# Kernel optimization log

Hardware: AMD Instinct MI355X
Metric: run time of the kernel (lower is better)

Reference implementation:

```python
import jax, jax.numpy as jnp
import numpy as np

EPS = 1e-5

def batchnorm2d(x, gamma, beta):
    # training-mode BN over (N, T, V) per channel; x: [N, C, T, V]
    mean = jnp.mean(x, axis=(0, 2, 3), keepdims=True)
    var = jnp.var(x, axis=(0, 2, 3), keepdims=True)
    xhat = (x - mean) * jax.lax.rsqrt(var + EPS)
    return xhat * gamma[None, :, None, None] + beta[None, :, None, None]

def temporal_shift(x, theta, stride):
    # learnable per-channel temporal shift with linear interpolation, zero pad
    # x: [N, C, T, V], theta: [C]
    N, C, T, V = x.shape
    T_out = T // stride
    t = jnp.arange(T_out, dtype=theta.dtype)
    pos = t[None, :] * stride + theta[:, None]          # [C, T_out]
    i0 = jnp.floor(pos).astype(jnp.int32)
    frac = (pos - i0.astype(theta.dtype))[None, :, :, None]  # [1,C,T_out,1]
    cidx = jnp.arange(C)[:, None]                        # [C, 1]

    def gather(idx):
        valid = (idx >= 0) & (idx < T)
        g = x[:, cidx, jnp.clip(idx, 0, T - 1), :]       # [N, C, T_out, V]
        return jnp.where(valid[None, :, :, None], g, 0.0)

    return gather(i0) * (1.0 - frac) + gather(i0 + 1) * frac

def setup_inputs() -> dict:
    key = jax.random.key(0)
    k = jax.random.split(key, 6)
    N, Cin, Cout, T, V = 64, 256, 256, 64, 25
    x = jax.random.normal(k[0], (N, Cin, T, V), dtype=jnp.float32)
    # kaiming normal fan_out for 1x1 conv: std = sqrt(2 / (Cout*1*1))
    conv_w = jax.random.normal(k[1], (Cout, Cin), dtype=jnp.float32) * np.float32(np.sqrt(2.0 / Cout))
    conv_b = jnp.zeros((Cout,), dtype=jnp.float32)
    bn1_g = jnp.ones((Cin,), dtype=jnp.float32)
    bn1_b = jnp.zeros((Cin,), dtype=jnp.float32)
    bn2_g = jnp.ones((Cin,), dtype=jnp.float32)   # bn_init(bn2, 1)
    bn2_b = jnp.zeros((Cin,), dtype=jnp.float32)
    theta_in = jax.random.uniform(k[2], (Cin,), jnp.float32, -1.0, 1.0)
    theta_out = jax.random.uniform(k[3], (Cout,), jnp.float32, -1.0, 1.0)
    return {"x": x, "conv_w": conv_w, "conv_b": conv_b,
            "bn1_g": bn1_g, "bn1_b": bn1_b, "bn2_g": bn2_g, "bn2_b": bn2_b,
            "theta_in": theta_in, "theta_out": theta_out}

def reference(x, conv_w, conv_b, bn1_g, bn1_b, bn2_g, bn2_b, theta_in, theta_out):
    stride = 1
    h = batchnorm2d(x, bn1_g, bn1_b)
    h = temporal_shift(h, theta_in, 1)
    h = jnp.einsum('nctv,oc->notv', h, conv_w) + conv_b[None, :, None, None]
    h = jax.nn.relu(h)
    h = temporal_shift(h, theta_out, stride)
    h = batchnorm2d(h, bn2_g, bn2_b)
    return h
```

## Files before the change

kernel.cpp:

```cpp
#include <hip/hip_runtime.h>


#define EPSV 1e-5f
constexpr int Nn = 64, Cc = 256, Tt = 64, Vv = 25;
constexpr int TV = Tt * Vv;
constexpr int CTV = Cc * TV;
constexpr float Minv = 1.0f / (Nn * TV);

typedef short short8 __attribute__((ext_vector_type(8)));
typedef float floatx4 __attribute__((ext_vector_type(4)));

__device__ __forceinline__ unsigned short f2bf(float f) {
    unsigned int u = __builtin_bit_cast(unsigned int, f);
    u += 0x7FFFu + ((u >> 16) & 1u);
    return (unsigned short)(u >> 16);
}
__device__ __forceinline__ float bflo(unsigned int w) {
    return __builtin_bit_cast(float, w << 16);
}
__device__ __forceinline__ float bfhi(unsigned int w) {
    return __builtin_bit_cast(float, w & 0xFFFF0000u);
}
__device__ __forceinline__ void unp8v(uint4 u, float* o) {
    o[0] = bflo(u.x); o[1] = bfhi(u.x); o[2] = bflo(u.y); o[3] = bfhi(u.y);
    o[4] = bflo(u.z); o[5] = bfhi(u.z); o[6] = bflo(u.w); o[7] = bfhi(u.w);
}
__device__ __forceinline__ void gload_lds16(const void* g, void* l) {
    __builtin_amdgcn_global_load_lds((const __attribute__((address_space(1))) void*)g,
                                     (__attribute__((address_space(3))) void*)l, 16, 0, 0);
}

__global__ __launch_bounds__(256) void k_stats_shift(const float* __restrict__ x,
                                                     const float* __restrict__ theta,
                                                     float* __restrict__ sacc,
                                                     float* __restrict__ qacc,
                                                     unsigned short* __restrict__ ht) {
    int c0 = blockIdx.x * 64;
    int E0 = blockIdx.y * 200;
    int n  = blockIdx.z;
    int tid = threadIdx.x;
    __shared__ __attribute__((aligned(16))) unsigned short xt[256][70];
    __shared__ int   pd[64];
    __shared__ float pf[64];
    if (tid < 64) {
        float th = theta[c0 + tid];
        float fd = floorf(th);
        pd[tid] = (int)fd;
        pf[tid] = th - fd;
    }
    int lo = E0 - 28; if (lo < 0) lo = 0;
    int hi = E0 + 228; if (hi > 1600) hi = 1600;
    int ldsoff = lo - (E0 - 28);
    int nf4 = (hi - lo) >> 2;
    {
        int cp = tid >> 3, li = tid & 7;
        int ca = 2 * cp;
        const float4* xr0 = (const float4*)(x + (size_t)n * CTV + (size_t)(c0 + ca) * TV + lo);
        const float4* xr1 = xr0 + (TV >> 2);
        float s0 = 0.f, q0 = 0.f, s1 = 0.f, q1 = 0.f;
        float4 acur = xr0[li], bcur = xr1[li];
#pragma unroll
        for (int s = 0; s < 8; ++s) {
            int i = li + s * 8;
            int inx = i + 8;
            float4 anxt, bnxt;
            if (inx < nf4) { anxt = xr0[inx]; bnxt = xr1[inx]; }
            if (i < nf4) {
                int r = ldsoff + i * 4;
#pragma unroll
                for (int k = 0; k < 4; ++k) {
                    float a = ((const float*)&acur)[k];
                    float b = ((const float*)&bcur)[k];
                    if ((unsigned)(r + k - 28) < 200u) {
                        s0 += a; q0 += a * a; s1 += b; q1 += b * b;
                    }
                    unsigned int pk = (unsigned int)f2bf(a) | (((unsigned int)f2bf(b)) << 16);
                    *(unsigned int*)&xt[r + k][ca] = pk;
                }
            }
            acur = anxt; bcur = bnxt;
        }
        for (int off = 4; off; off >>= 1) {
            s0 += __shfl_down(s0, off); q0 += __shfl_down(q0, off);
            s1 += __shfl_down(s1, off); q1 += __shfl_down(q1, off);
        }
        if (li == 0) {
            atomicAdd(&sacc[c0 + ca], s0);     atomicAdd(&qacc[c0 + ca], q0);
            atomicAdd(&sacc[c0 + ca + 1], s1); atomicAdd(&qacc[c0 + ca + 1], q1);
        }
    }
    __syncthreads();
    int cseg = tid & 7, er = tid >> 3;
    int cb = cseg * 8;
    int dk[8]; float fk[8];
#pragma unroll
    for (int k = 0; k < 8; ++k) { dk[k] = pd[cb + k]; fk[k] = pf[cb + k]; }
    for (int it = 0; it < 7; ++it) {
        int tv_l = er + it * 32;
        if (tv_l >= 200) break;
        int e = E0 + tv_l;
        float A8[8], B8[8], C8[8];
        {
            const unsigned short* rA = &xt[tv_l + 3][cb];
            const unsigned short* rB = &xt[tv_l + 28][cb];
            const unsigned short* rC = &xt[tv_l + 53][cb];
            uint2 a0 = *(const uint2*)rA, a1 = *(const uint2*)(rA + 4);
            uint2 b0 = *(const uint2*)rB, b1 = *(const uint2*)(rB + 4);
            uint2 g0 = *(const uint2*)rC, g1 = *(const uint2*)(rC + 4);
            A8[0]=bflo(a0.x); A8[1]=bfhi(a0.x); A8[2]=bflo(a0.y); A8[3]=bfhi(a0.y);
            A8[4]=bflo(a1.x); A8[5]=bfhi(a1.x); A8[6]=bflo(a1.y); A8[7]=bfhi(a1.y);
            B8[0]=bflo(b0.x); B8[1]=bfhi(b0.x); B8[2]=bflo(b0.y); B8[3]=bfhi(b0.y);
            B8[4]=bflo(b1.x); B8[5]=bfhi(b1.x); B8[6]=bflo(b1.y); B8[7]=bfhi(b1.y);
            C8[0]=bflo(g0.x); C8[1]=bfhi(g0.x); C8[2]=bflo(g0.y); C8[3]=bfhi(g0.y);
            C8[4]=bflo(g1.x); C8[5]=bfhi(g1.x); C8[6]=bflo(g1.y); C8[7]=bfhi(g1.y);
        }
        unsigned int w4[4];
#pragma unroll
        for (int k = 0; k < 8; ++k) {
            int d = dk[k]; float f = fk[k];
            float x0 = (d < 0) ? A8[k] : B8[k];
            float x1 = (d < 0) ? B8[k] : C8[k];
            int e0 = e + 25 * d;
            float v0 = ((unsigned)e0 < 1600u) ? x0 : 0.f;
            float v1 = ((unsigned)(e0 + 25) < 1600u) ? x1 : 0.f;
            unsigned short hb = f2bf(v0 + f * (v1 - v0));
            if (k & 1) w4[k >> 1] |= ((unsigned int)hb) << 16;
            else       w4[k >> 1] = hb;
        }
        uint4 st = { w4[0], w4[1], w4[2], w4[3] };
        *(uint4*)(ht + (size_t)(n * 1600 + e) * 256 + c0 + cb) = st;
    }
}

__global__ __launch_bounds__(256) void k_params(const float* __restrict__ w,
                                                const float* __restrict__ bias,
                                                const float* __restrict__ sacc,
                                                const float* __restrict__ qacc,
                                                const float* __restrict__ g,
                                                const float* __restrict__ b,
                                                const float* __restrict__ theta,
                                                unsigned short* __restrict__ wb,
                                                float* __restrict__ b2all,
                                                float* __restrict__ s0v,
                                                float* __restrict__ s63v) {
    int o = blockIdx.x, c = threadIdx.x;
    float mean = sacc[c] * Minv;
    float var  = qacc[c] * Minv - mean * mean;
    float sc = g[c] * rsqrtf(var + EPSV);
    float tc = b[c] - mean * sc;
    float th = theta[c];
    float fd = floorf(th);
    int d = (int)fd;
    float f = th - fd;
    float wv = w[o * 256 + c];
    wb[o * 256 + c] = f2bf(wv * sc);
    float wtc = wv * tc;
    float r0  = (d < 0) ? wtc * (1.f - f) : 0.f;
    float r63 = (d == 0) ? wtc * f : 0.f;
    for (int off = 32; off; off >>= 1) {
        wtc += __shfl_down(wtc, off);
        r0  += __shfl_down(r0, off);
        r63 += __shfl_down(r63, off);
    }
    __shared__ float aux[3][4];
    if ((c & 63) == 0) { int wi = c >> 6; aux[0][wi] = wtc; aux[1][wi] = r0; aux[2][wi] = r63; }
    __syncthreads();
    if (c == 0) {
        b2all[o] = bias[o] + aux[0][0] + aux[0][1] + aux[0][2] + aux[0][3];
        s0v[o]  = aux[1][0] + aux[1][1] + aux[1][2] + aux[1][3];
        s63v[o] = aux[2][0] + aux[2][1] + aux[2][2] + aux[2][3];
    }
}

__global__ __launch_bounds__(256, 2) void k_gemm(const unsigned short* __restrict__ ht,
                                                 const unsigned short* __restrict__ wb,
                                                 const float* __restrict__ b2all,
                                                 const float* __restrict__ s0v,
                                                 const float* __restrict__ s63v,
                                                 unsigned short* __restrict__ y) {
    int j0 = blockIdx.x * 128;
    int tid = threadIdx.x;
    int w = tid >> 6, lane = tid & 63;
    int quad = lane >> 4, l16 = lane & 15;
    __shared__ __attribute__((aligned(16))) unsigned short smem[36864];
    floatx4 acc[4][8] = {};
    int sg = (lane & 3) ^ ((lane >> 3) & 3);
    const unsigned short* wpA = wb + (size_t)(w * 64 + (lane >> 2)) * 256 + sg * 8;
    const unsigned short* hpB = ht + (size_t)(j0 + w * 32 + (lane >> 2)) * 256 + sg * 8;
    int rg = quad ^ ((l16 >> 1) & 3);

#define STAGE(buf, k0)                                                              \
    {                                                                               \
        unsigned short* Ab_ = smem + (buf) * 12288;                                 \
        unsigned short* Bb_ = Ab_ + 8192;                                           \
        _Pragma("unroll")                                                           \
        for (int a = 0; a < 4; ++a)                                                 \
            gload_lds16(wpA + (size_t)a * 16 * 256 + (k0), Ab_ + (w * 64 + a * 16) * 32); \
        _Pragma("unroll")                                                           \
        for (int b = 0; b < 2; ++b)                                                 \
            gload_lds16(hpB + (size_t)b * 16 * 256 + (k0), Bb_ + (w * 32 + b * 16) * 32); \
    }
#define COMPUTE(buf)                                                                \
    {                                                                               \
        const unsigned short* Ab_ = smem + (buf) * 12288;                           \
        const unsigned short* Bb_ = Ab_ + 8192;                                     \
        short8 af[4];                                                               \
        _Pragma("unroll")                                                           \
        for (int m = 0; m < 4; ++m)                                                 \
            af[m] = *(const short8*)&Ab_[(w * 64 + m * 16 + l16) * 32 + rg * 8];    \
        __builtin_amdgcn_s_setprio(1);                                              \
        _Pragma("unroll")                                                           \
        for (int jt = 0; jt < 8; ++jt) {                                            \
            short8 bfr = *(const short8*)&Bb_[(jt * 16 + l16) * 32 + rg * 8];       \
            _Pragma("unroll")                                                       \
            for (int m = 0; m < 4; ++m)                                             \
                acc[m][jt] = __builtin_amdgcn_mfma_f32_16x16x32_bf16(af[m], bfr, acc[m][jt], 0, 0, 0); \
        }                                                                           \
        __builtin_amdgcn_s_setprio(0);                                              \
    }
#define WAITVM(n) asm volatile("s_waitcnt vmcnt(" #n ")" ::: "memory")
#define BAR() __builtin_amdgcn_s_barrier()

    STAGE(0, 0)
    STAGE(1, 32)
    WAITVM(6); BAR();
    STAGE(2, 64)
    COMPUTE(0)
    WAITVM(6); BAR();
    STAGE(0, 96)
    COMPUTE(1)
    WAITVM(6); BAR();
    STAGE(1, 128)
    COMPUTE(2)
    WAITVM(6); BAR();
    STAGE(2, 160)
    COMPUTE(0)
    WAITVM(6); BAR();
    STAGE(0, 192)
    COMPUTE(1)
    WAITVM(6); BAR();
    STAGE(1, 224)
    COMPUTE(2)
    WAITVM(6); BAR();
    COMPUTE(0)
    WAITVM(0); BAR();
    COMPUTE(1)
#undef STAGE
#undef COMPUTE
#undef WAITVM
#undef BAR

    __syncthreads();
    unsigned short* Cl = smem;
    int li = tid & 15, orow = tid >> 4;
#pragma unroll
    for (int p = 0; p < 2; ++p) {
        if ((w >> 1) == p) {
            int rowbase = (w & 1) * 64;
#pragma unroll
            for (int m = 0; m < 4; ++m) {
                int ob = p * 128 + (w & 1) * 64 + m * 16 + quad * 4;
#pragma unroll
                for (int r = 0; r < 4; ++r) {
                    int o = ob + r;
                    float bb = b2all[o], e0 = s0v[o], e63 = s63v[o];
                    int lrow = rowbase + m * 16 + quad * 4 + r;
#pragma unroll
                    for (int jt = 0; jt < 8; ++jt) {
                        int jj = j0 + jt * 16;
                        int nn = jj / 1600;
                        int tvb = jj - nn * 1600 + l16;
                        float bia = bb - (tvb < 25 ? e0 : 0.f) - (tvb >= 1575 ? e63 : 0.f);
                        float v = acc[m][jt][r] + bia;
                        v = v > 0.f ? v : 0.f;
                        Cl[lrow * 136 + jt * 16 + l16] = f2bf(v);
                    }
                }
            }
        }
        __syncthreads();
#pragma unroll
        for (int pass = 0; pass < 8; ++pass) {
            int ol = orow + pass * 16;
            uint4 vv = *(const uint4*)&Cl[ol * 136 + li * 8];
            int o = p * 128 + ol;
            int j = j0 + li * 8;
            int nn = j / 1600;
            int tv = j - nn * 1600;
            *(uint4*)(y + (size_t)nn * CTV + (size_t)o * TV + tv) = vv;
        }
        if (p == 0) __syncthreads();
    }
}

__global__ __launch_bounds__(256) void k_bn2_stats(const unsigned short* __restrict__ y,
                                                   float* __restrict__ acc7) {
    int o = blockIdx.y, ng = blockIdx.x, tid = threadIdx.x;
    float S = 0.f, Q = 0.f, P = 0.f, Y0 = 0.f, Q0 = 0.f, Y63 = 0.f, Q63 = 0.f;
    if (tid < 200) {
        int e = tid * 8;
        int eB = e + 24; if (eB > 1592) eB = 1592;
        int eC = e + 32; if (eC > 1592) eC = 1592;
        const unsigned short* base0 = y + (size_t)(ng * 8) * CTV + (size_t)o * TV;
        uint4 ua = *(const uint4*)(base0 + e);
        uint4 ub = *(const uint4*)(base0 + eB);
        uint4 uc = *(const uint4*)(base0 + eC);
        for (int nn = 0; nn < 8; ++nn) {
            uint4 na, nb, nc;
            if (nn < 7) {
                const unsigned short* row = base0 + (size_t)(nn + 1) * CTV;
                na = *(const uint4*)(row + e);
                nb = *(const uint4*)(row + eB);
                nc = *(const uint4*)(row + eC);
            }
            float a[8], b[8], c[8];
            unp8v(ua, a); unp8v(ub, b); unp8v(uc, c);
#pragma unroll
            for (int k = 0; k < 8; ++k) {
                float v = a[k];
                S += v; Q += v * v;
                float vn = (k < 7) ? b[k + 1] : c[0];
                if (e + k < 1575) P += v * vn;
            }
            if (e < 32) {
#pragma unroll
                for (int k = 0; k < 8; ++k)
                    if (e + k < 25) { Y0 += a[k]; Q0 += a[k] * a[k]; }
            }
            if (e >= 1568) {
#pragma unroll
                for (int k = 0; k < 8; ++k)
                    if (e + k >= 1575) { Y63 += a[k]; Q63 += a[k] * a[k]; }
            }
            ua = na; ub = nb; uc = nc;
        }
    }
    for (int off = 32; off; off >>= 1) {
        S += __shfl_down(S, off); Q += __shfl_down(Q, off); P += __shfl_down(P, off);
        Y0 += __shfl_down(Y0, off); Q0 += __shfl_down(Q0, off);
        Y63 += __shfl_down(Y63, off); Q63 += __shfl_down(Q63, off);
    }
    if ((tid & 63) == 0) {
        atomicAdd(&acc7[o], S);           atomicAdd(&acc7[256 + o], Q);
        atomicAdd(&acc7[512 + o], P);     atomicAdd(&acc7[768 + o], Y0);
        atomicAdd(&acc7[1024 + o], Q0);   atomicAdd(&acc7[1280 + o], Y63);
        atomicAdd(&acc7[1536 + o], Q63);
    }
}

__global__ __launch_bounds__(256) void k_bn2_apply(const unsigned short* __restrict__ y,
                                                   const float* __restrict__ theta,
                                                   const float* __restrict__ acc7,
                                                   const float* __restrict__ g,
                                                   const float* __restrict__ b,
                                                   float* __restrict__ out) {
    int o = blockIdx.y, n = blockIdx.x, tid = threadIdx.x;
    float th = theta[o];
    float fd = floorf(th);
    int d = (int)fd;
    float f = th - fd;
    float S = acc7[o], Q = acc7[256 + o], P = acc7[512 + o];
    float Y0 = acc7[768 + o], Q0 = acc7[1024 + o], Y63 = acc7[1280 + o], Q63 = acc7[1536 + o];
    float omf = 1.f - f;
    float sz, qz;
    if (d < 0) { sz = S - omf * Y63; qz = omf * omf * (Q - Q63) + f * f * Q + 2.f * f * omf * P; }
    else       { sz = S - f * Y0;    qz = omf * omf * Q + f * f * (Q - Q0) + 2.f * f * omf * P; }
    float mean = sz * Minv;
    float var = qz * Minv - mean * mean;
    float sc = g[o] * rsqrtf(var + EPSV);
    float tc = b[o] - mean * sc;
    if (tid >= 200) return;
    int e = tid * 8;
    const unsigned short* row = y + (size_t)n * CTV + (size_t)o * TV;
    float a0[8], a1[8];
    if (d < 0) {
        int eA = e - 32; if (eA < 0) eA = 0;
        int eB = e - 24; if (eB < 0) eB = 0;
        float A[8], B[8], M[8];
        unp8v(*(const uint4*)(row + eA), A);
        unp8v(*(const uint4*)(row + eB), B);
        unp8v(*(const uint4*)(row + e), M);
        a0[0] = (e >= 25) ? A[7] : 0.f;
#pragma unroll
        for (int k = 1; k < 8; ++k) a0[k] = (e + k >= 25) ? B[k - 1] : 0.f;
#pragma unroll
        for (int k = 0; k < 8; ++k) a1[k] = M[k];
    } else {
        int eB = e + 24; if (eB > 1592) eB = 1592;
        int eC = e + 32; if (eC > 1592) eC = 1592;
        float M[8], B[8], C[8];
        unp8v(*(const uint4*)(row + e), M);
        unp8v(*(const uint4*)(row + eB), B);
        unp8v(*(const uint4*)(row + eC), C);
#pragma unroll
        for (int k = 0; k < 8; ++k) a0[k] = M[k];
#pragma unroll
        for (int k = 0; k < 7; ++k) a1[k] = (e + k < 1575) ? B[k + 1] : 0.f;
        a1[7] = (e + 7 < 1575) ? C[0] : 0.f;
    }
    float4 r0, r1;
#pragma unroll
    for (int k = 0; k < 4; ++k) {
        ((float*)&r0)[k] = (omf * a0[k] + f * a1[k]) * sc + tc;
        ((float*)&r1)[k] = (omf * a0[k + 4] + f * a1[k + 4]) * sc + tc;
    }
    float* op = out + (size_t)n * CTV + (size_t)o * TV + e;
    *(float4*)op = r0;
    *(float4*)(op + 4) = r1;
}

extern "C" void kernel_launch(void* const* d_in, const int* in_sizes, int n_in,
                              void* d_out, int out_size, void* d_ws, size_t ws_size,
                              hipStream_t stream) {
    const float* x      = (const float*)d_in[0];
    const float* conv_w = (const float*)d_in[1];
    const float* conv_b = (const float*)d_in[2];
    const float* bn1_g  = (const float*)d_in[3];
    const float* bn1_b  = (const float*)d_in[4];
    const float* bn2_g  = (const float*)d_in[5];
    const float* bn2_b  = (const float*)d_in[6];
    const float* th_in  = (const float*)d_in[7];
    const float* th_out = (const float*)d_in[8];
    float* out = (float*)d_out;

    char* ws = (char*)d_ws;
    unsigned short* ht = (unsigned short*)ws;
    unsigned short* yy = (unsigned short*)(ws + 52428800);
    unsigned short* wb = (unsigned short*)(ws + 104857600);
    float* sacc1 = (float*)(ws + 104988672);
    float* qacc1 = sacc1 + 256;
    float* acc7  = qacc1 + 256;
    float* b2all = acc7 + 7 * 256;
    float* s0v   = b2all + 256;
    float* s63v  = s0v + 256;

    hipMemsetAsync((void*)sacc1, 0, 9 * 256 * sizeof(float), stream);
    hipLaunchKernelGGL(k_stats_shift, dim3(4, 8, 64), dim3(256), 0, stream,
                       x, th_in, sacc1, qacc1, ht);
    hipLaunchKernelGGL(k_params, dim3(256), dim3(256), 0, stream,
                       conv_w, conv_b, sacc1, qacc1, bn1_g, bn1_b, th_in,
                       wb, b2all, s0v, s63v);
    hipLaunchKernelGGL(k_gemm, dim3(800), dim3(256), 0, stream,
                       ht, wb, b2all, s0v, s63v, yy);
    hipLaunchKernelGGL(k_bn2_stats, dim3(8, 256), dim3(256), 0, stream, yy, acc7);
    hipLaunchKernelGGL(k_bn2_apply, dim3(64, 256), dim3(256), 0, stream,
                       yy, th_out, acc7, bn2_g, bn2_b, out);
}
```

Measured before the change: 347.1 us.

## Store shifted activations channel-major and transpose via ds_read_b64_tr_b16 in GEMM

The first kernel no longer transposes x through LDS into a [n,tv,c] bf16 buffer. It streams each (n,c) row directly, applies the temporal shift with neighbouring global loads, and writes a channel-major [c, n*tv] bf16 buffer. The GEMM then loads B tiles from that layout and transposes them on the fly with ds_read_b64_tr_b16 LDS reads. The goal is to drop the LDS transpose and its strided writes from the stats/shift stage. The cost is more redundant global reads for the shift neighbours and a more complex inline-asm B-fragment path in the GEMM.

```diff
diff --git a/kernel.cpp b/kernel.cpp
--- a/kernel.cpp
+++ b/kernel.cpp
@@ -5,10 +5,13 @@
 constexpr int Nn = 64, Cc = 256, Tt = 64, Vv = 25;
 constexpr int TV = Tt * Vv;
 constexpr int CTV = Cc * TV;
+constexpr int NJ = Nn * TV;
 constexpr float Minv = 1.0f / (Nn * TV);
 
 typedef short short8 __attribute__((ext_vector_type(8)));
 typedef float floatx4 __attribute__((ext_vector_type(4)));
+typedef unsigned int uintx2 __attribute__((ext_vector_type(2)));
+typedef unsigned int uintx4 __attribute__((ext_vector_type(4)));
 
 __device__ __forceinline__ unsigned short f2bf(float f) {
     unsigned int u = __builtin_bit_cast(unsigned int, f);
@@ -30,105 +33,68 @@
                                      (__attribute__((address_space(3))) void*)l, 16, 0, 0);
 }
 
-__global__ __launch_bounds__(256) void k_stats_shift(const float* __restrict__ x,
-                                                     const float* __restrict__ theta,
-                                                     float* __restrict__ sacc,
-                                                     float* __restrict__ qacc,
-                                                     unsigned short* __restrict__ ht) {
-    int c0 = blockIdx.x * 64;
-    int E0 = blockIdx.y * 200;
-    int n  = blockIdx.z;
-    int tid = threadIdx.x;
-    __shared__ __attribute__((aligned(16))) unsigned short xt[256][70];
-    __shared__ int   pd[64];
-    __shared__ float pf[64];
-    if (tid < 64) {
-        float th = theta[c0 + tid];
-        float fd = floorf(th);
-        pd[tid] = (int)fd;
-        pf[tid] = th - fd;
-    }
-    int lo = E0 - 28; if (lo < 0) lo = 0;
-    int hi = E0 + 228; if (hi > 1600) hi = 1600;
-    int ldsoff = lo - (E0 - 28);
-    int nf4 = (hi - lo) >> 2;
-    {
-        int cp = tid >> 3, li = tid & 7;
-        int ca = 2 * cp;
-        const float4* xr0 = (const float4*)(x + (size_t)n * CTV + (size_t)(c0 + ca) * TV + lo);
-        const float4* xr1 = xr0 + (TV >> 2);
-        float s0 = 0.f, q0 = 0.f, s1 = 0.f, q1 = 0.f;
-        float4 acur = xr0[li], bcur = xr1[li];
-#pragma unroll
-        for (int s = 0; s < 8; ++s) {
-            int i = li + s * 8;
-            int inx = i + 8;
-            float4 anxt, bnxt;
-            if (inx < nf4) { anxt = xr0[inx]; bnxt = xr1[inx]; }
-            if (i < nf4) {
-                int r = ldsoff + i * 4;
-#pragma unroll
-                for (int k = 0; k < 4; ++k) {
-                    float a = ((const float*)&acur)[k];
-                    float b = ((const float*)&bcur)[k];
-                    if ((unsigned)(r + k - 28) < 200u) {
-                        s0 += a; q0 += a * a; s1 += b; q1 += b * b;
-                    }
-                    unsigned int pk = (unsigned int)f2bf(a) | (((unsigned int)f2bf(b)) << 16);
-                    *(unsigned int*)&xt[r + k][ca] = pk;
-                }
-            }
-            acur = anxt; bcur = bnxt;
-        }
-        for (int off = 4; off; off >>= 1) {
-            s0 += __shfl_down(s0, off); q0 += __shfl_down(q0, off);
-            s1 += __shfl_down(s1, off); q1 += __shfl_down(q1, off);
-        }
-        if (li == 0) {
-            atomicAdd(&sacc[c0 + ca], s0);     atomicAdd(&qacc[c0 + ca], q0);
-            atomicAdd(&sacc[c0 + ca + 1], s1); atomicAdd(&qacc[c0 + ca + 1], q1);
-        }
-    }
-    __syncthreads();
-    int cseg = tid & 7, er = tid >> 3;
-    int cb = cseg * 8;
-    int dk[8]; float fk[8];
-#pragma unroll
-    for (int k = 0; k < 8; ++k) { dk[k] = pd[cb + k]; fk[k] = pf[cb + k]; }
-    for (int it = 0; it < 7; ++it) {
-        int tv_l = er + it * 32;
-        if (tv_l >= 200) break;
-        int e = E0 + tv_l;
-        float A8[8], B8[8], C8[8];
-        {
-            const unsigned short* rA = &xt[tv_l + 3][cb];
-            const unsigned short* rB = &xt[tv_l + 28][cb];
-            const unsigned short* rC = &xt[tv_l + 53][cb];
-            uint2 a0 = *(const uint2*)rA, a1 = *(const uint2*)(rA + 4);
-            uint2 b0 = *(const uint2*)rB, b1 = *(const uint2*)(rB + 4);
-            uint2 g0 = *(const uint2*)rC, g1 = *(const uint2*)(rC + 4);
-            A8[0]=bflo(a0.x); A8[1]=bfhi(a0.x); A8[2]=bflo(a0.y); A8[3]=bfhi(a0.y);
-            A8[4]=bflo(a1.x); A8[5]=bfhi(a1.x); A8[6]=bflo(a1.y); A8[7]=bfhi(a1.y);
-            B8[0]=bflo(b0.x); B8[1]=bfhi(b0.x); B8[2]=bflo(b0.y); B8[3]=bfhi(b0.y);
-            B8[4]=bflo(b1.x); B8[5]=bfhi(b1.x); B8[6]=bflo(b1.y); B8[7]=bfhi(b1.y);
-            C8[0]=bflo(g0.x); C8[1]=bfhi(g0.x); C8[2]=bflo(g0.y); C8[3]=bfhi(g0.y);
-            C8[4]=bflo(g1.x); C8[5]=bfhi(g1.x); C8[6]=bflo(g1.y); C8[7]=bfhi(g1.y);
+__global__ __launch_bounds__(256) void k_bn1_stream(const float* __restrict__ x,
+                                                    const float* __restrict__ theta,
+                                                    float* __restrict__ sacc,
+                                                    float* __restrict__ qacc,
+                                                    unsigned short* __restrict__ ht2) {
+    int n = blockIdx.x, c = blockIdx.y, tid = threadIdx.x;
+    const float* xr = x + (size_t)n * CTV + (size_t)c * TV;
+    float th = theta[c];
+    float fd = floorf(th);
+    int d = (int)fd;
+    float f = th - fd, omf = 1.f - f;
+    float s = 0.f, q = 0.f;
+    if (tid < 200) {
+        int e = tid * 8;
+        float4 m0 = *(const float4*)(xr + e);
+        float4 m1 = *(const float4*)(xr + e + 4);
+        float M[8] = {m0.x, m0.y, m0.z, m0.w, m1.x, m1.y, m1.z, m1.w};
+#pragma unroll
+        for (int k = 0; k < 8; ++k) { s += M[k]; q += M[k] * M[k]; }
+        float out[8];
+        if (d < 0) {
+            int b0 = e - 28; if (b0 < 0) b0 = 0;
+            int b1 = e - 24; if (b1 < 0) b1 = 0;
+            int b2 = e - 20; if (b2 < 0) b2 = 0;
+            float4 l0 = *(const float4*)(xr + b0);
+            float4 l1 = *(const float4*)(xr + b1);
+            float4 l2 = *(const float4*)(xr + b2);
+            float S[8] = { l0.w, l1.x, l1.y, l1.z, l1.w, l2.x, l2.y, l2.z };
+#pragma unroll
+            for (int k = 0; k < 8; ++k) {
+                float v0 = (e + k >= 25) ? S[k] : 0.f;
+                out[k] = omf * v0 + f * M[k];
+            }
+        } else {
+            int b0 = e + 24; if (b0 > 1596) b0 = 1596;
+            int b1 = e + 28; if (b1 > 1596) b1 = 1596;
+            int b2 = e + 32; if (b2 > 1596) b2 = 1596;
+            float4 l0 = *(const float4*)(xr + b0);
+            float4 l1 = *(const float4*)(xr + b1);
+            float4 l2 = *(const float4*)(xr + b2);
+            float S[8] = { l0.y, l0.z, l0.w, l1.x, l1.y, l1.z, l1.w, l2.x };
+#pragma unroll
+            for (int k = 0; k < 8; ++k) {
+                float v1 = (e + k < 1575) ? S[k] : 0.f;
+                out[k] = omf * M[k] + f * v1;
+            }
         }
         unsigned int w4[4];
 #pragma unroll
-        for (int k = 0; k < 8; ++k) {
-            int d = dk[k]; float f = fk[k];
-            float x0 = (d < 0) ? A8[k] : B8[k];
-            float x1 = (d < 0) ? B8[k] : C8[k];
-            int e0 = e + 25 * d;
-            float v0 = ((unsigned)e0 < 1600u) ? x0 : 0.f;
-            float v1 = ((unsigned)(e0 + 25) < 1600u) ? x1 : 0.f;
-            unsigned short hb = f2bf(v0 + f * (v1 - v0));
-            if (k & 1) w4[k >> 1] |= ((unsigned int)hb) << 16;
-            else       w4[k >> 1] = hb;
-        }
+        for (int k = 0; k < 8; k += 2)
+            w4[k >> 1] = (unsigned)f2bf(out[k]) | (((unsigned)f2bf(out[k + 1])) << 16);
         uint4 st = { w4[0], w4[1], w4[2], w4[3] };
-        *(uint4*)(ht + (size_t)(n * 1600 + e) * 256 + c0 + cb) = st;
+        *(uint4*)(ht2 + (size_t)c * NJ + n * TV + e) = st;
+    }
+    for (int off = 32; off; off >>= 1) { s += __shfl_down(s, off); q += __shfl_down(q, off); }
+    __shared__ float red[8];
+    int wv = tid >> 6;
+    if ((tid & 63) == 0) { red[wv] = s; red[4 + wv] = q; }
+    __syncthreads();
+    if (tid == 0) {
+        atomicAdd(&sacc[c], red[0] + red[1] + red[2] + red[3]);
+        atomicAdd(&qacc[c], red[4] + red[5] + red[6] + red[7]);
     }
 }
 
@@ -172,7 +138,7 @@
     }
 }
 
-__global__ __launch_bounds__(256, 2) void k_gemm(const unsigned short* __restrict__ ht,
+__global__ __launch_bounds__(256, 2) void k_gemm(const unsigned short* __restrict__ ht2,
                                                  const unsigned short* __restrict__ wb,
                                                  const float* __restrict__ b2all,
                                                  const float* __restrict__ s0v,
@@ -186,60 +152,105 @@
     floatx4 acc[4][8] = {};
     int sg = (lane & 3) ^ ((lane >> 3) & 3);
     const unsigned short* wpA = wb + (size_t)(w * 64 + (lane >> 2)) * 256 + sg * 8;
-    const unsigned short* hpB = ht + (size_t)(j0 + w * 32 + (lane >> 2)) * 256 + sg * 8;
     int rg = quad ^ ((l16 >> 1) & 3);
-
-#define STAGE(buf, k0)                                                              \
-    {                                                                               \
-        unsigned short* Ab_ = smem + (buf) * 12288;                                 \
-        unsigned short* Bb_ = Ab_ + 8192;                                           \
-        _Pragma("unroll")                                                           \
-        for (int a = 0; a < 4; ++a)                                                 \
-            gload_lds16(wpA + (size_t)a * 16 * 256 + (k0), Ab_ + (w * 64 + a * 16) * 32); \
-        _Pragma("unroll")                                                           \
-        for (int b = 0; b < 2; ++b)                                                 \
-            gload_lds16(hpB + (size_t)b * 16 * 256 + (k0), Bb_ + (w * 32 + b * 16) * 32); \
-    }
-#define COMPUTE(buf)                                                                \
-    {                                                                               \
-        const unsigned short* Ab_ = smem + (buf) * 12288;                           \
-        const unsigned short* Bb_ = Ab_ + 8192;                                     \
-        short8 af[4];                                                               \
-        _Pragma("unroll")                                                           \
-        for (int m = 0; m < 4; ++m)                                                 \
-            af[m] = *(const short8*)&Ab_[(w * 64 + m * 16 + l16) * 32 + rg * 8];    \
-        __builtin_amdgcn_s_setprio(1);                                              \
-        _Pragma("unroll")                                                           \
-        for (int jt = 0; jt < 8; ++jt) {                                            \
-            short8 bfr = *(const short8*)&Bb_[(jt * 16 + l16) * 32 + rg * 8];       \
-            _Pragma("unroll")                                                       \
-            for (int m = 0; m < 4; ++m)                                             \
-                acc[m][jt] = __builtin_amdgcn_mfma_f32_16x16x32_bf16(af[m], bfr, acc[m][jt], 0, 0, 0); \
-        }                                                                           \
-        __builtin_amdgcn_s_setprio(0);                                              \
+    int brow0 = w * 8 + ((lane & 7) >> 1);
+    int bcol  = (lane >> 3) * 16 + (lane & 1) * 8;
+    const unsigned short* hp0 = ht2 + (size_t)brow0 * NJ + j0 + bcol;
+    const unsigned short* hp1 = hp0 + (size_t)4 * NJ;
+    unsigned trlane = (unsigned)(quad * 2048 + l16 * 8);
+
+#define STAGE(buf, kt)                                                                  \
+    {                                                                                   \
+        unsigned short* Ab_ = smem + (buf) * 12288;                                     \
+        unsigned short* Bb_ = Ab_ + 8192;                                               \
+        _Pragma("unroll")                                                               \
+        for (int a = 0; a < 4; ++a)                                                     \
+            gload_lds16(wpA + (size_t)a * 16 * 256 + (kt) * 32, Ab_ + (w * 64 + a * 16) * 32); \
+        gload_lds16(hp0 + (size_t)(kt) * (32 * (size_t)NJ), Bb_ + (w * 2) * 512);       \
+        gload_lds16(hp1 + (size_t)(kt) * (32 * (size_t)NJ), Bb_ + (w * 2 + 1) * 512);   \
+    }
+#define COMPUTE(buf)                                                                    \
+    {                                                                                   \
+        const unsigned short* Ab_ = smem + (buf) * 12288;                               \
+        unsigned ba = (unsigned)(size_t)(const void*)(Ab_ + 8192) + trlane;             \
+        short8 af[4];                                                                   \
+        _Pragma("unroll")                                                               \
+        for (int m = 0; m < 4; ++m)                                                     \
+            af[m] = *(const short8*)&Ab_[(w * 64 + m * 16 + l16) * 32 + rg * 8];        \
+        uintx2 t0_, t1_, t2_, t3_, t4_, t5_, t6_, t7_;                                  \
+        uintx2 u0_, u1_, u2_, u3_, u4_, u5_, u6_, u7_;                                  \
+        asm volatile("ds_read_b64_tr_b16 %0, %2 offset:0\n\t"                           \
+                     "ds_read_b64_tr_b16 %1, %2 offset:1024"                            \
+                     : "=v"(t0_), "=v"(u0_) : "v"(ba));                                 \
+        asm volatile("ds_read_b64_tr_b16 %0, %2 offset:0\n\t"                           \
+                     "ds_read_b64_tr_b16 %1, %2 offset:1024"                            \
+                     : "=v"(t1_), "=v"(u1_) : "v"(ba + 128));                           \
+        asm volatile("ds_read_b64_tr_b16 %0, %2 offset:0\n\t"                           \
+                     "ds_read_b64_tr_b16 %1, %2 offset:1024"                            \
+                     : "=v"(t2_), "=v"(u2_) : "v"(ba + 256));                           \
+        asm volatile("ds_read_b64_tr_b16 %0, %2 offset:0\n\t"                           \
+                     "ds_read_b64_tr_b16 %1, %2 offset:1024"                            \
+                     : "=v"(t3_), "=v"(u3_) : "v"(ba + 384));                           \
+        asm volatile("ds_read_b64_tr_b16 %0, %2 offset:0\n\t"                           \
+                     "ds_read_b64_tr_b16 %1, %2 offset:1024"                            \
+                     : "=v"(t4_), "=v"(u4_) : "v"(ba + 512));                           \
+        asm volatile("ds_read_b64_tr_b16 %0, %2 offset:0\n\t"                           \
+                     "ds_read_b64_tr_b16 %1, %2 offset:1024"                            \
+                     : "=v"(t5_), "=v"(u5_) : "v"(ba + 640));                           \
+        asm volatile("ds_read_b64_tr_b16 %0, %2 offset:0\n\t"                           \
+                     "ds_read_b64_tr_b16 %1, %2 offset:1024"                            \
+                     : "=v"(t6_), "=v"(u6_) : "v"(ba + 768));                           \
+        asm volatile("ds_read_b64_tr_b16 %0, %2 offset:0\n\t"                           \
+                     "ds_read_b64_tr_b16 %1, %2 offset:1024"                            \
+                     : "=v"(t7_), "=v"(u7_) : "v"(ba + 896));                           \
+        asm volatile("s_waitcnt lgkmcnt(0)" ::: "memory");                              \
+        __builtin_amdgcn_sched_barrier(0);                                              \
+        __builtin_amdgcn_s_setprio(1);                                                  \
+        uintx4 uu;                                                                      \
+        short8 bfr;                                                                     \
+        _Pragma("unroll")                                                               \
+        for (int m = 0; m < 4; ++m) {                                                   \
+            uu = (uintx4){t0_.x, t0_.y, u0_.x, u0_.y}; bfr = __builtin_bit_cast(short8, uu); \
+            acc[m][0] = __builtin_amdgcn_mfma_f32_16x16x32_bf16(af[m], bfr, acc[m][0], 0, 0, 0); \
+            uu = (uintx4){t1_.x, t1_.y, u1_.x, u1_.y}; bfr = __builtin_bit_cast(short8, uu); \
+            acc[m][1] = __builtin_amdgcn_mfma_f32_16x16x32_bf16(af[m], bfr, acc[m][1], 0, 0, 0); \
+            uu = (uintx4){t2_.x, t2_.y, u2_.x, u2_.y}; bfr = __builtin_bit_cast(short8, uu); \
+            acc[m][2] = __builtin_amdgcn_mfma_f32_16x16x32_bf16(af[m], bfr, acc[m][2], 0, 0, 0); \
+            uu = (uintx4){t3_.x, t3_.y, u3_.x, u3_.y}; bfr = __builtin_bit_cast(short8, uu); \
+            acc[m][3] = __builtin_amdgcn_mfma_f32_16x16x32_bf16(af[m], bfr, acc[m][3], 0, 0, 0); \
+            uu = (uintx4){t4_.x, t4_.y, u4_.x, u4_.y}; bfr = __builtin_bit_cast(short8, uu); \
+            acc[m][4] = __builtin_amdgcn_mfma_f32_16x16x32_bf16(af[m], bfr, acc[m][4], 0, 0, 0); \
+            uu = (uintx4){t5_.x, t5_.y, u5_.x, u5_.y}; bfr = __builtin_bit_cast(short8, uu); \
+            acc[m][5] = __builtin_amdgcn_mfma_f32_16x16x32_bf16(af[m], bfr, acc[m][5], 0, 0, 0); \
+            uu = (uintx4){t6_.x, t6_.y, u6_.x, u6_.y}; bfr = __builtin_bit_cast(short8, uu); \
+            acc[m][6] = __builtin_amdgcn_mfma_f32_16x16x32_bf16(af[m], bfr, acc[m][6], 0, 0, 0); \
+            uu = (uintx4){t7_.x, t7_.y, u7_.x, u7_.y}; bfr = __builtin_bit_cast(short8, uu); \
+            acc[m][7] = __builtin_amdgcn_mfma_f32_16x16x32_bf16(af[m], bfr, acc[m][7], 0, 0, 0); \
+        }                                                                               \
+        __builtin_amdgcn_s_setprio(0);                                                  \
     }
 #define WAITVM(n) asm volatile("s_waitcnt vmcnt(" #n ")" ::: "memory")
 #define BAR() __builtin_amdgcn_s_barrier()
 
     STAGE(0, 0)
-    STAGE(1, 32)
-    WAITVM(6); BAR();
-    STAGE(2, 64)
+    STAGE(1, 1)
+    WAITVM(6); BAR();
+    STAGE(2, 2)
     COMPUTE(0)
     WAITVM(6); BAR();
-    STAGE(0, 96)
+    STAGE(0, 3)
     COMPUTE(1)
     WAITVM(6); BAR();
-    STAGE(1, 128)
+    STAGE(1, 4)
     COMPUTE(2)
     WAITVM(6); BAR();
-    STAGE(2, 160)
+    STAGE(2, 5)
     COMPUTE(0)
     WAITVM(6); BAR();
-    STAGE(0, 192)
+    STAGE(0, 6)
     COMPUTE(1)
     WAITVM(6); BAR();
-    STAGE(1, 224)
+    STAGE(1, 7)
     COMPUTE(2)
     WAITVM(6); BAR();
     COMPUTE(0)
@@ -424,7 +435,7 @@
     float* out = (float*)d_out;
 
     char* ws = (char*)d_ws;
-    unsigned short* ht = (unsigned short*)ws;
+    unsigned short* ht2 = (unsigned short*)ws;
     unsigned short* yy = (unsigned short*)(ws + 52428800);
     unsigned short* wb = (unsigned short*)(ws + 104857600);
     float* sacc1 = (float*)(ws + 104988672);
@@ -435,13 +446,13 @@
     float* s63v  = s0v + 256;
 
     hipMemsetAsync((void*)sacc1, 0, 9 * 256 * sizeof(float), stream);
-    hipLaunchKernelGGL(k_stats_shift, dim3(4, 8, 64), dim3(256), 0, stream,
-                       x, th_in, sacc1, qacc1, ht);
+    hipLaunchKernelGGL(k_bn1_stream, dim3(64, 256), dim3(256), 0, stream,
+                       x, th_in, sacc1, qacc1, ht2);
     hipLaunchKernelGGL(k_params, dim3(256), dim3(256), 0, stream,
                        conv_w, conv_b, sacc1, qacc1, bn1_g, bn1_b, th_in,
                        wb, b2all, s0v, s63v);
     hipLaunchKernelGGL(k_gemm, dim3(800), dim3(256), 0, stream,
-                       ht, wb, b2all, s0v, s63v, yy);
+                       ht2, wb, b2all, s0v, s63v, yy);
     hipLaunchKernelGGL(k_bn2_stats, dim3(8, 256), dim3(256), 0, stream, yy, acc7);
     hipLaunchKernelGGL(k_bn2_apply, dim3(64, 256), dim3(256), 0, stream,
                        yy, th_out, acc7, bn2_g, bn2_b, out);
```

New measurement: 347.4 us. About the same (+0.1%).
